# Optimization experiments

Measured on AMD Instinct MI355X. Metric: run time of the kernel, lower is better.

The kernel has to match this reference:

```python
import jax, jax.numpy as jnp
import numpy as np

N = 100000
IN_DIM = 256
HID = 256
EMB = 64
E = 3200000
EPS = 1e-3  # keras BatchNormalization default epsilon


def setup_inputs() -> dict:
    key = jax.random.key(0)
    ks = jax.random.split(key, 8)
    x = jax.random.normal(ks[0], (N, IN_DIM), dtype=jnp.float32)
    edge_row = jax.random.randint(ks[1], (E,), 0, N, dtype=jnp.int32)
    edge_col = jax.random.randint(ks[2], (E,), 0, N, dtype=jnp.int32)
    edge_val = jax.random.uniform(ks[3], (E,), dtype=jnp.float32)
    # glorot-uniform weights
    lim1 = float(np.sqrt(6.0 / (IN_DIM + HID)))
    w1 = jax.random.uniform(ks[4], (IN_DIM, HID), minval=-lim1, maxval=lim1, dtype=jnp.float32)
    lim2 = float(np.sqrt(6.0 / (HID + EMB)))
    w2 = jax.random.uniform(ks[5], (HID, EMB), minval=-lim2, maxval=lim2, dtype=jnp.float32)
    # BN params (inference mode uses moving stats)
    gamma1 = jnp.ones((HID,), jnp.float32)
    beta1 = jnp.zeros((HID,), jnp.float32)
    mean1 = jax.random.normal(ks[6], (HID,), dtype=jnp.float32) * 0.1
    var1 = jnp.ones((HID,), jnp.float32)
    gamma2 = jnp.ones((EMB,), jnp.float32)
    beta2 = jnp.zeros((EMB,), jnp.float32)
    mean2 = jax.random.normal(ks[7], (EMB,), dtype=jnp.float32) * 0.1
    var2 = jnp.ones((EMB,), jnp.float32)
    return dict(x=x, edge_row=edge_row, edge_col=edge_col, edge_val=edge_val,
                w1=w1, w2=w2, gamma1=gamma1, beta1=beta1, mean1=mean1, var1=var1,
                gamma2=gamma2, beta2=beta2, mean2=mean2, var2=var2)


def _spmm(edge_row, edge_col, edge_val, dense):
    # out[i] = sum_{e: row_e == i} val_e * dense[col_e]
    gathered = edge_val[:, None] * dense[edge_col]  # [E, D]
    return jax.ops.segment_sum(gathered, edge_row, num_segments=N)


def _bn_inf(h, gamma, beta, mean, var):
    return (h - mean) * jax.lax.rsqrt(var + EPS) * gamma + beta


def reference(x, edge_row, edge_col, edge_val, w1, w2,
              gamma1, beta1, mean1, var1, gamma2, beta2, mean2, var2):
    # layer 1: A @ (X W1), BN (inference), ReLU; dropout is identity at inference
    h = _spmm(edge_row, edge_col, edge_val, x @ w1)
    h = jax.nn.relu(_bn_inf(h, gamma1, beta1, mean1, var1))
    # layer 2
    z = _spmm(edge_row, edge_col, edge_val, h @ w2)
    z = _bn_inf(z, gamma2, beta2, mean2, var2)
    return z
```

## Files before the change

### kernel.cpp

```cpp
#include <hip/hip_runtime.h>
#include <hip/hip_bf16.h>

constexpr int NN   = 100000;
constexpr int IND  = 256;
constexpr int HIDD = 256;
constexpr int EMBD = 64;
constexpr int EE   = 3200000;
constexpr int CB    = 8;
constexpr int NB    = ((NN - 1) >> CB) + 1;
constexpr int NBP   = 512;
constexpr int CHUNK = 4096;
constexpr int EPT   = CHUNK / 256;
constexpr int NCHUNK = (EE + CHUNK - 1) / CHUNK;
constexpr int GMT    = 8;
constexpr int GROWS  = GMT * 16;
constexpr int GGRID  = (NN + GROWS - 1) / GROWS;
constexpr int APITCH = 264;
#define EPS_BN 1e-3f

typedef short  short8  __attribute__((ext_vector_type(8)));
typedef float  floatx4 __attribute__((ext_vector_type(4)));
typedef float  floatx2 __attribute__((ext_vector_type(2)));

static __device__ __forceinline__ unsigned short f2bf(float f) {
  __hip_bfloat16 b = __float2bfloat16(f);
  union { __hip_bfloat16 b; unsigned short u; } cv;
  cv.b = b;
  return cv.u;
}
static __device__ __forceinline__ float bf2f(unsigned short u) {
  return __uint_as_float(((unsigned)u) << 16);
}
static __device__ __forceinline__ unsigned char f2fp8(float f) {
  return (unsigned char)__builtin_amdgcn_cvt_pk_fp8_f32(f, f, 0, false);
}

__global__ __launch_bounds__(256) void swz_w1_kernel(
    const float* __restrict__ w1, unsigned short* __restrict__ w1s) {
  const int t = blockIdx.x * blockDim.x + threadIdx.x;
  const int lane = t & 63;
  const int f = t >> 6;
  const int kt = f >> 4;
  const int nt = f & 15;
  const int n = nt * 16 + (lane & 15);
#pragma unroll
  for (int j = 0; j < 8; ++j) {
    const int k = kt * 32 + (lane >> 4) * 8 + j;
    w1s[(size_t)(f * 64 + lane) * 8 + j] = f2bf(w1[k * HIDD + n]);
  }
}

__global__ __launch_bounds__(256) void swz_w2_kernel(
    const float* __restrict__ w2, unsigned short* __restrict__ w2s) {
  const int t = blockIdx.x * blockDim.x + threadIdx.x;
  const int lane = t & 63;
  const int f = t >> 6;
  const int kt = f >> 2;
  const int nt = f & 3;
  const int n = nt * 16 + (lane & 15);
#pragma unroll
  for (int j = 0; j < 8; ++j) {
    const int k = kt * 32 + (lane >> 4) * 8 + j;
    w2s[(size_t)(f * 64 + lane) * 8 + j] = f2bf(w2[k * EMBD + n]);
  }
}

__global__ __launch_bounds__(512) void gemm1_mfma(
    const float* __restrict__ x, const unsigned short* __restrict__ w1s,
    unsigned char* __restrict__ h0) {
  __shared__ unsigned short sa[2][16][APITCH];
  const int tid  = threadIdx.x;
  const int lane = tid & 63;
  const int wave = tid >> 6;
  const int quad = lane >> 4;
  const int l15  = lane & 15;
  const short8* w1v = (const short8*)w1s;
  short8 bf[2][8];
#pragma unroll
  for (int nt2 = 0; nt2 < 2; ++nt2)
#pragma unroll
    for (int kt = 0; kt < 8; ++kt)
      bf[nt2][kt] = w1v[(size_t)(kt * 16 + wave * 2 + nt2) * 64 + lane];

  const int mbase = blockIdx.x * GROWS;
  const int srow = tid >> 5;
  const int scol = (tid & 31) * 8;

  auto srcp = [&](int mt) -> const float* {
    int r = mbase + mt * 16 + srow;
    if (r >= NN) r = NN - 1;
    return x + (size_t)r * IND + scol;
  };

  {
    const float* p = srcp(0);
    float4 g0 = *(const float4*)(p);
    float4 g1 = *(const float4*)(p + 4);
    short8 s;
    s[0] = (short)f2bf(g0.x); s[1] = (short)f2bf(g0.y);
    s[2] = (short)f2bf(g0.z); s[3] = (short)f2bf(g0.w);
    s[4] = (short)f2bf(g1.x); s[5] = (short)f2bf(g1.y);
    s[6] = (short)f2bf(g1.z); s[7] = (short)f2bf(g1.w);
    *(short8*)&sa[0][srow][(tid & 31) * 8] = s;
  }

#pragma unroll
  for (int mt = 0; mt < GMT; ++mt) {
    const int cur = mt & 1;
    float4 g0, g1;
    if (mt + 1 < GMT) {
      const float* p = srcp(mt + 1);
      g0 = *(const float4*)(p);
      g1 = *(const float4*)(p + 4);
    }
    __syncthreads();
    floatx4 c0 = {0.f, 0.f, 0.f, 0.f};
    floatx4 c1 = {0.f, 0.f, 0.f, 0.f};
#pragma unroll
    for (int kt = 0; kt < 8; ++kt) {
      short8 a = *(const short8*)&sa[cur][l15][quad * 8 + kt * 32];
      c0 = __builtin_amdgcn_mfma_f32_16x16x32_bf16(a, bf[0][kt], c0, 0, 0, 0);
      c1 = __builtin_amdgcn_mfma_f32_16x16x32_bf16(a, bf[1][kt], c1, 0, 0, 0);
    }
    const int m0 = mbase + mt * 16;
    if (m0 < NN) {
      unsigned char* o = h0 + (size_t)(m0 + quad * 4) * HIDD + wave * 32 + l15;
#pragma unroll
      for (int r = 0; r < 4; ++r) {
        o[(size_t)r * HIDD]      = f2fp8(c0[r]);
        o[(size_t)r * HIDD + 16] = f2fp8(c1[r]);
      }
    }
    if (mt + 1 < GMT) {
      short8 s;
      s[0] = (short)f2bf(g0.x); s[1] = (short)f2bf(g0.y);
      s[2] = (short)f2bf(g0.z); s[3] = (short)f2bf(g0.w);
      s[4] = (short)f2bf(g1.x); s[5] = (short)f2bf(g1.y);
      s[6] = (short)f2bf(g1.z); s[7] = (short)f2bf(g1.w);
      *(short8*)&sa[cur ^ 1][srow][(tid & 31) * 8] = s;
    }
  }
}

__global__ __launch_bounds__(256) void gemm2_mfma(
    const unsigned short* __restrict__ hb, const unsigned short* __restrict__ w2s,
    unsigned char* __restrict__ z0) {
  __shared__ unsigned short sa[2][16][APITCH];
  const int tid  = threadIdx.x;
  const int lane = tid & 63;
  const int wave = tid >> 6;
  const int quad = lane >> 4;
  const int l15  = lane & 15;
  const short8* w2v = (const short8*)w2s;
  short8 bf[8];
#pragma unroll
  for (int kt = 0; kt < 8; ++kt)
    bf[kt] = w2v[(size_t)(kt * 4 + wave) * 64 + lane];

  const int mbase = blockIdx.x * GROWS;
  const int srow = tid >> 4;
  const int scol = (tid & 15) * 16;

  auto srcp = [&](int mt) -> const unsigned short* {
    int r = mbase + mt * 16 + srow;
    if (r >= NN) r = NN - 1;
    return hb + (size_t)r * HIDD + scol;
  };

  {
    const unsigned short* p = srcp(0);
    short8 g0 = *(const short8*)(p);
    short8 g1 = *(const short8*)(p + 8);
    *(short8*)&sa[0][srow][scol]     = g0;
    *(short8*)&sa[0][srow][scol + 8] = g1;
  }

#pragma unroll
  for (int mt = 0; mt < GMT; ++mt) {
    const int cur = mt & 1;
    short8 g0, g1;
    if (mt + 1 < GMT) {
      const unsigned short* p = srcp(mt + 1);
      g0 = *(const short8*)(p);
      g1 = *(const short8*)(p + 8);
    }
    __syncthreads();
    floatx4 c = {0.f, 0.f, 0.f, 0.f};
#pragma unroll
    for (int kt = 0; kt < 8; ++kt) {
      short8 a = *(const short8*)&sa[cur][l15][quad * 8 + kt * 32];
      c = __builtin_amdgcn_mfma_f32_16x16x32_bf16(a, bf[kt], c, 0, 0, 0);
    }
    const int m0 = mbase + mt * 16;
    if (m0 < NN) {
      unsigned char* o = z0 + (size_t)(m0 + quad * 4) * EMBD + wave * 16 + l15;
#pragma unroll
      for (int r = 0; r < 4; ++r) o[(size_t)r * EMBD] = f2fp8(c[r]);
    }
    if (mt + 1 < GMT) {
      *(short8*)&sa[cur ^ 1][srow][scol]     = g0;
      *(short8*)&sa[cur ^ 1][srow][scol + 8] = g1;
    }
  }
}

__global__ __launch_bounds__(256) void histb_kernel(
    const int* __restrict__ row, int* __restrict__ bcnt) {
  __shared__ int lcnt[NB];
  for (int i = threadIdx.x; i < NB; i += 256) lcnt[i] = 0;
  __syncthreads();
  const int base = blockIdx.x * CHUNK;
  const int lim  = min(EE - base, CHUNK);
  for (int i = threadIdx.x; i < lim; i += 256)
    atomicAdd(&lcnt[row[base + i] >> CB], 1);
  __syncthreads();
  for (int i = threadIdx.x; i < NB; i += 256) {
    const int c = lcnt[i];
    if (c) atomicAdd(&bcnt[i * 16], c);
  }
}

__global__ __launch_bounds__(512) void bscan_kernel(
    const int* __restrict__ bcnt, int* __restrict__ bucket_start,
    int* __restrict__ bcur) {
  __shared__ int lds[512];
  int v = (threadIdx.x < NB) ? bcnt[threadIdx.x * 16] : 0;
  lds[threadIdx.x] = v;
  for (int off = 1; off < 512; off <<= 1) {
    __syncthreads();
    int t = (threadIdx.x >= off) ? lds[threadIdx.x - off] : 0;
    __syncthreads();
    lds[threadIdx.x] += t;
  }
  __syncthreads();
  if (threadIdx.x < NB) {
    const int excl = lds[threadIdx.x] - v;
    bucket_start[threadIdx.x] = excl;
    bcur[threadIdx.x * 16] = excl;
  }
  if (threadIdx.x == 0) bucket_start[NB] = EE;
}

__global__ __launch_bounds__(256) void partA_kernel(
    const int* __restrict__ row, const int* __restrict__ col,
    const float* __restrict__ val, int* __restrict__ bcur,
    unsigned long long* __restrict__ staged) {
  __shared__ unsigned long long sbuf[CHUNK];
  __shared__ int cnt[NBP];
  __shared__ int scn[NBP];
  __shared__ int cur[NB];
  __shared__ int gofs[NB];
  const int base = blockIdx.x * CHUNK;
  const int lim  = min(EE - base, CHUNK);
  for (int i = threadIdx.x; i < NBP; i += 256) cnt[i] = 0;
  __syncthreads();
  unsigned long long rec[EPT];
  int bkt[EPT];
#pragma unroll
  for (int j = 0; j < EPT; ++j) {
    const int idx = threadIdx.x + j * 256;
    bkt[j] = -1;
    if (idx < lim) {
      const int e = base + idx;
      const int r = row[e];
      const int c = col[e];
      const unsigned short v = f2bf(val[e]);
      rec[j] = ((unsigned long long)r << 33) | ((unsigned long long)c << 16) | v;
      bkt[j] = r >> CB;
      atomicAdd(&cnt[bkt[j]], 1);
    }
  }
  __syncthreads();
  for (int i = threadIdx.x; i < NBP; i += 256) scn[i] = cnt[i];
  __syncthreads();
  for (int off = 1; off < NBP; off <<= 1) {
    const int i0 = threadIdx.x, i1 = threadIdx.x + 256;
    const int t0 = (i0 >= off) ? scn[i0 - off] : 0;
    const int t1 = (i1 >= off) ? scn[i1 - off] : 0;
    __syncthreads();
    scn[i0] += t0;
    scn[i1] += t1;
    __syncthreads();
  }
  for (int b = threadIdx.x; b < NB; b += 256) cur[b] = scn[b] - cnt[b];
  __syncthreads();
#pragma unroll
  for (int j = 0; j < EPT; ++j)
    if (bkt[j] >= 0) {
      const int p = atomicAdd(&cur[bkt[j]], 1);
      sbuf[p] = rec[j];
    }
  __syncthreads();
  for (int b = threadIdx.x; b < NB; b += 256) {
    const int c = cnt[b];
    const int g = (c > 0) ? atomicAdd(&bcur[b * 16], c) : 0;
    gofs[b] = g - (scn[b] - c);
  }
  __syncthreads();
  for (int s = threadIdx.x; s < lim; s += 256) {
    const unsigned long long rc = sbuf[s];
    const int b = (int)(rc >> (33 + CB));
    staged[(size_t)(gofs[b] + s)] = rc;
  }
}

__global__ __launch_bounds__(256) void partB_kernel(
    const int* __restrict__ bucket_start,
    const unsigned long long* __restrict__ staged,
    int2* __restrict__ edges, int* __restrict__ row_start) {
  __shared__ int cnt[1 << CB];
  __shared__ int ofs[1 << CB];
  const int b  = blockIdx.x;
  const int r0 = b << CB;
  const int rn = min(NN - r0, 1 << CB);
  const int s  = bucket_start[b];
  const int e  = bucket_start[b + 1];
  cnt[threadIdx.x] = 0;
  __syncthreads();
  const unsigned* hi = (const unsigned*)staged;
  for (int p = s + threadIdx.x; p < e; p += 256) {
    const unsigned hw = hi[2 * p + 1];
    const int r = (int)((hw >> 1) & 0x1FFFF);
    atomicAdd(&cnt[r - r0], 1);
  }
  __syncthreads();
  const int v = cnt[threadIdx.x];
  ofs[threadIdx.x] = v;
  for (int off = 1; off < 256; off <<= 1) {
    __syncthreads();
    const int t = (threadIdx.x >= off) ? ofs[threadIdx.x - off] : 0;
    __syncthreads();
    ofs[threadIdx.x] += t;
  }
  __syncthreads();
  const int excl = ofs[threadIdx.x] - v;
  if ((int)threadIdx.x < rn) row_start[r0 + threadIdx.x] = s + excl;
  if (b == NB - 1 && threadIdx.x == 0) row_start[NN] = e;
  __syncthreads();
  cnt[threadIdx.x] = s + excl;
  __syncthreads();
  for (int p = s + threadIdx.x; p < e; p += 256) {
    const unsigned long long rc = staged[p];
    const int r = (int)(rc >> 33);
    const int c = (int)((rc >> 16) & 0x1FFFF);
    const float vv = bf2f((unsigned short)(rc & 0xFFFF));
    const int q = atomicAdd(&cnt[r - r0], 1);
    int2 pk; pk.x = c << 6; pk.y = __float_as_int(vv);
    edges[q] = pk;
  }
}

__global__ __launch_bounds__(256, 8) void spmm1_kernel(
    const unsigned char* __restrict__ h0, const int* __restrict__ row_start,
    const int2* __restrict__ edges,
    const float* __restrict__ gamma, const float* __restrict__ beta,
    const float* __restrict__ mean, const float* __restrict__ var,
    unsigned short* __restrict__ h) {
  const int row  = (blockIdx.x * blockDim.x + threadIdx.x) >> 6;
  const int lane = threadIdx.x & 63;
  const int grp  = lane >> 4;
  const int t    = lane & 15;
  const int t16  = t * 16;
  const int s = row_start[row];
  const int e = row_start[row + 1];
  floatx2 acc[8];
#pragma unroll
  for (int j = 0; j < 8; ++j) acc[j] = floatx2{0.f, 0.f};

  const int ebulk = s + ((e - s) & ~15);
  int p = s;
  for (; p < ebulk; p += 16) {
    unsigned coff[4];
    float    vv4[4];
#pragma unroll
    for (int k = 0; k < 4; ++k) {
      const int2 er = edges[p + k * 4 + grp];
      coff[k] = (unsigned)er.x;
      vv4[k]  = __int_as_float(er.y);
    }
    uint4 gg[4];
#pragma unroll
    for (int k = 0; k < 4; ++k)
      gg[k] = *(const uint4*)(h0 + (size_t)coff[k] * 4 + t16);
#pragma unroll
    for (int k = 0; k < 4; ++k) {
      const floatx2 v2 = {vv4[k], vv4[k]};
      acc[0] += __builtin_amdgcn_cvt_pk_f32_fp8(gg[k].x, false) * v2;
      acc[1] += __builtin_amdgcn_cvt_pk_f32_fp8(gg[k].x, true)  * v2;
      acc[2] += __builtin_amdgcn_cvt_pk_f32_fp8(gg[k].y, false) * v2;
      acc[3] += __builtin_amdgcn_cvt_pk_f32_fp8(gg[k].y, true)  * v2;
      acc[4] += __builtin_amdgcn_cvt_pk_f32_fp8(gg[k].z, false) * v2;
      acc[5] += __builtin_amdgcn_cvt_pk_f32_fp8(gg[k].z, true)  * v2;
      acc[6] += __builtin_amdgcn_cvt_pk_f32_fp8(gg[k].w, false) * v2;
      acc[7] += __builtin_amdgcn_cvt_pk_f32_fp8(gg[k].w, true)  * v2;
    }
  }
  for (; p < e; p += 4) {
    const int idx = p + grp;
    const bool valid = idx < e;
    const int2 er = edges[valid ? idx : e - 1];
    const unsigned coff = (unsigned)er.x;
    const float vv = valid ? __int_as_float(er.y) : 0.f;
    const uint4 gg = *(const uint4*)(h0 + (size_t)coff * 4 + t16);
    const floatx2 v2 = {vv, vv};
    acc[0] += __builtin_amdgcn_cvt_pk_f32_fp8(gg.x, false) * v2;
    acc[1] += __builtin_amdgcn_cvt_pk_f32_fp8(gg.x, true)  * v2;
    acc[2] += __builtin_amdgcn_cvt_pk_f32_fp8(gg.y, false) * v2;
    acc[3] += __builtin_amdgcn_cvt_pk_f32_fp8(gg.y, true)  * v2;
    acc[4] += __builtin_amdgcn_cvt_pk_f32_fp8(gg.z, false) * v2;
    acc[5] += __builtin_amdgcn_cvt_pk_f32_fp8(gg.z, true)  * v2;
    acc[6] += __builtin_amdgcn_cvt_pk_f32_fp8(gg.w, false) * v2;
    acc[7] += __builtin_amdgcn_cvt_pk_f32_fp8(gg.w, true)  * v2;
  }
#pragma unroll
  for (int j = 0; j < 8; ++j) {
    acc[j][0] += __shfl_xor(acc[j][0], 16);
    acc[j][1] += __shfl_xor(acc[j][1], 16);
  }
#pragma unroll
  for (int j = 0; j < 8; ++j) {
    acc[j][0] += __shfl_xor(acc[j][0], 32);
    acc[j][1] += __shfl_xor(acc[j][1], 32);
  }
  floatx2 pa, pb;
  if (grp == 0)      { pa = acc[0]; pb = acc[1]; }
  else if (grp == 1) { pa = acc[2]; pb = acc[3]; }
  else if (grp == 2) { pa = acc[4]; pb = acc[5]; }
  else               { pa = acc[6]; pb = acc[7]; }
  const int d = t16 + grp * 4;
  float4 g  = *(const float4*)(gamma + d);
  float4 b  = *(const float4*)(beta + d);
  float4 m  = *(const float4*)(mean + d);
  float4 vv = *(const float4*)(var + d);
  const unsigned short o0 =
      f2bf(fmaxf(fmaf((pa[0] - m.x) * rsqrtf(vv.x + EPS_BN), g.x, b.x), 0.f));
  const unsigned short o1 =
      f2bf(fmaxf(fmaf((pa[1] - m.y) * rsqrtf(vv.y + EPS_BN), g.y, b.y), 0.f));
  const unsigned short o2 =
      f2bf(fmaxf(fmaf((pb[0] - m.z) * rsqrtf(vv.z + EPS_BN), g.z, b.z), 0.f));
  const unsigned short o3 =
      f2bf(fmaxf(fmaf((pb[1] - m.w) * rsqrtf(vv.w + EPS_BN), g.w, b.w), 0.f));
  const unsigned long long ow =
      (unsigned long long)o0 | ((unsigned long long)o1 << 16) |
      ((unsigned long long)o2 << 32) | ((unsigned long long)o3 << 48);
  __builtin_nontemporal_store(
      ow, (unsigned long long*)(h + (size_t)row * HIDD + d));
}

__global__ __launch_bounds__(256, 8) void spmm2_kernel(
    const unsigned char* __restrict__ z0, const int* __restrict__ row_start,
    const int2* __restrict__ edges,
    const float* __restrict__ gamma, const float* __restrict__ beta,
    const float* __restrict__ mean, const float* __restrict__ var,
    float* __restrict__ out) {
  const int row  = (blockIdx.x * blockDim.x + threadIdx.x) >> 6;
  const int lane = threadIdx.x & 63;
  const int grp  = lane >> 4;
  const int t    = lane & 15;
  const int t4   = t * 4;
  const int s = row_start[row];
  const int e = row_start[row + 1];
  floatx2 a01 = {0.f, 0.f};
  floatx2 a23 = {0.f, 0.f};
  const int ebulk = s + ((e - s) & ~15);
  int p = s;
  for (; p < ebulk; p += 16) {
    unsigned coff[4];
    float    vv4[4];
#pragma unroll
    for (int k = 0; k < 4; ++k) {
      const int2 er = edges[p + k * 4 + grp];
      coff[k] = (unsigned)er.x;
      vv4[k]  = __int_as_float(er.y);
    }
    unsigned gg[4];
#pragma unroll
    for (int k = 0; k < 4; ++k)
      gg[k] = *(const unsigned*)(z0 + (size_t)coff[k] + t4);
#pragma unroll
    for (int k = 0; k < 4; ++k) {
      const floatx2 v2 = {vv4[k], vv4[k]};
      a01 += __builtin_amdgcn_cvt_pk_f32_fp8(gg[k], false) * v2;
      a23 += __builtin_amdgcn_cvt_pk_f32_fp8(gg[k], true)  * v2;
    }
  }
  for (; p < e; p += 4) {
    const int idx = p + grp;
    const bool valid = idx < e;
    const int2 er = edges[valid ? idx : e - 1];
    const unsigned coff = (unsigned)er.x;
    const float vvs = valid ? __int_as_float(er.y) : 0.f;
    const unsigned gg = *(const unsigned*)(z0 + (size_t)coff + t4);
    const floatx2 v2 = {vvs, vvs};
    a01 += __builtin_amdgcn_cvt_pk_f32_fp8(gg, false) * v2;
    a23 += __builtin_amdgcn_cvt_pk_f32_fp8(gg, true)  * v2;
  }
  a01[0] += __shfl_xor(a01[0], 16); a01[1] += __shfl_xor(a01[1], 16);
  a23[0] += __shfl_xor(a23[0], 16); a23[1] += __shfl_xor(a23[1], 16);
  a01[0] += __shfl_xor(a01[0], 32); a01[1] += __shfl_xor(a01[1], 32);
  a23[0] += __shfl_xor(a23[0], 32); a23[1] += __shfl_xor(a23[1], 32);
  float av;
  if (grp == 0)      av = a01[0];
  else if (grp == 1) av = a01[1];
  else if (grp == 2) av = a23[0];
  else               av = a23[1];
  const int d = t4 + grp;
  const float r = fmaf((av - mean[d]) * rsqrtf(var[d] + EPS_BN), gamma[d],
                       beta[d]);
  __builtin_nontemporal_store(r, out + (size_t)row * EMBD + d);
}

extern "C" void kernel_launch(void* const* d_in, const int* in_sizes, int n_in,
                              void* d_out, int out_size, void* d_ws, size_t ws_size,
                              hipStream_t stream) {
  const float* x        = (const float*)d_in[0];
  const int*   edge_row = (const int*)d_in[1];
  const int*   edge_col = (const int*)d_in[2];
  const float* edge_val = (const float*)d_in[3];
  const float* w1       = (const float*)d_in[4];
  const float* w2       = (const float*)d_in[5];
  const float* gamma1   = (const float*)d_in[6];
  const float* beta1    = (const float*)d_in[7];
  const float* mean1    = (const float*)d_in[8];
  const float* var1     = (const float*)d_in[9];
  const float* gamma2   = (const float*)d_in[10];
  const float* beta2    = (const float*)d_in[11];
  const float* mean2    = (const float*)d_in[12];
  const float* var2     = (const float*)d_in[13];
  float* out = (float*)d_out;

  char* ws = (char*)d_ws;
  size_t off = 0;
  auto alloc = [&](size_t bytes) -> void* {
    void* p = ws + off;
    off = (off + bytes + 255) & ~(size_t)255;
    return p;
  };
  unsigned char*  h0  = (unsigned char*)alloc((size_t)NN * HIDD);
  unsigned short* h   = (unsigned short*)alloc((size_t)NN * HIDD * 2);
  unsigned long long* staged = (unsigned long long*)h;
  unsigned char*  z0  = (unsigned char*)alloc((size_t)NN * EMBD);
  unsigned short* w1s = (unsigned short*)alloc((size_t)IND * HIDD * 2);
  unsigned short* w2s = (unsigned short*)alloc((size_t)HIDD * EMBD * 2);
  int*   row_start    = (int*)alloc((size_t)(NN + 1) * 4);
  int*   bcnt         = (int*)alloc((size_t)NB * 16 * 4);
  int*   bcur         = (int*)alloc((size_t)NB * 16 * 4);
  int*   bucket_start = (int*)alloc((size_t)(NB + 1) * 4);
  int2*  edges        = (int2*)alloc((size_t)EE * 8);

  swz_w1_kernel<<<8192 / 256, 256, 0, stream>>>(w1, w1s);
  swz_w2_kernel<<<2048 / 256, 256, 0, stream>>>(w2, w2s);

  hipMemsetAsync(bcnt, 0, (size_t)NB * 16 * 4, stream);
  histb_kernel<<<NCHUNK, 256, 0, stream>>>(edge_row, bcnt);
  bscan_kernel<<<1, 512, 0, stream>>>(bcnt, bucket_start, bcur);
  partA_kernel<<<NCHUNK, 256, 0, stream>>>(
      edge_row, edge_col, edge_val, bcur, staged);
  partB_kernel<<<NB, 256, 0, stream>>>(bucket_start, staged, edges, row_start);

  gemm1_mfma<<<GGRID, 512, 0, stream>>>(x, w1s, h0);
  spmm1_kernel<<<NN / 4, 256, 0, stream>>>(h0, row_start, edges,
                                           gamma1, beta1, mean1, var1, h);
  gemm2_mfma<<<GGRID, 256, 0, stream>>>(h, w2s, z0);
  spmm2_kernel<<<NN / 4, 256, 0, stream>>>(z0, row_start, edges,
                                           gamma2, beta2, mean2, var2, out);
}
```

Measured before the change: 515.2 us.

## Fuse second-layer GEMM into first SpMM epilogue via shared-memory MFMA

The first SpMM kernel now has each wave aggregate four rows, apply BN+ReLU, and write bf16 results into a 16-row shared tile. The block then multiplies that tile by W2 with MFMA and writes fp8 z0 directly. This removes the separate gemm2 kernel and the round trip of the bf16 hidden matrix through global memory. The cost is lower occupancy (launch bound drops from 8 to 6, more registers held for W2 fragments) and serial per-wave row processing, which may hurt latency hiding in the gather.

```diff
diff --git a/kernel.cpp b/kernel.cpp
--- a/kernel.cpp
+++ b/kernel.cpp
@@ -142,68 +142,6 @@
   }
 }
 
-__global__ __launch_bounds__(256) void gemm2_mfma(
-    const unsigned short* __restrict__ hb, const unsigned short* __restrict__ w2s,
-    unsigned char* __restrict__ z0) {
-  __shared__ unsigned short sa[2][16][APITCH];
-  const int tid  = threadIdx.x;
-  const int lane = tid & 63;
-  const int wave = tid >> 6;
-  const int quad = lane >> 4;
-  const int l15  = lane & 15;
-  const short8* w2v = (const short8*)w2s;
-  short8 bf[8];
-#pragma unroll
-  for (int kt = 0; kt < 8; ++kt)
-    bf[kt] = w2v[(size_t)(kt * 4 + wave) * 64 + lane];
-
-  const int mbase = blockIdx.x * GROWS;
-  const int srow = tid >> 4;
-  const int scol = (tid & 15) * 16;
-
-  auto srcp = [&](int mt) -> const unsigned short* {
-    int r = mbase + mt * 16 + srow;
-    if (r >= NN) r = NN - 1;
-    return hb + (size_t)r * HIDD + scol;
-  };
-
-  {
-    const unsigned short* p = srcp(0);
-    short8 g0 = *(const short8*)(p);
-    short8 g1 = *(const short8*)(p + 8);
-    *(short8*)&sa[0][srow][scol]     = g0;
-    *(short8*)&sa[0][srow][scol + 8] = g1;
-  }
-
-#pragma unroll
-  for (int mt = 0; mt < GMT; ++mt) {
-    const int cur = mt & 1;
-    short8 g0, g1;
-    if (mt + 1 < GMT) {
-      const unsigned short* p = srcp(mt + 1);
-      g0 = *(const short8*)(p);
-      g1 = *(const short8*)(p + 8);
-    }
-    __syncthreads();
-    floatx4 c = {0.f, 0.f, 0.f, 0.f};
-#pragma unroll
-    for (int kt = 0; kt < 8; ++kt) {
-      short8 a = *(const short8*)&sa[cur][l15][quad * 8 + kt * 32];
-      c = __builtin_amdgcn_mfma_f32_16x16x32_bf16(a, bf[kt], c, 0, 0, 0);
-    }
-    const int m0 = mbase + mt * 16;
-    if (m0 < NN) {
-      unsigned char* o = z0 + (size_t)(m0 + quad * 4) * EMBD + wave * 16 + l15;
-#pragma unroll
-      for (int r = 0; r < 4; ++r) o[(size_t)r * EMBD] = f2fp8(c[r]);
-    }
-    if (mt + 1 < GMT) {
-      *(short8*)&sa[cur ^ 1][srow][scol]     = g0;
-      *(short8*)&sa[cur ^ 1][srow][scol + 8] = g1;
-    }
-  }
-}
-
 __global__ __launch_bounds__(256) void histb_kernel(
     const int* __restrict__ row, int* __restrict__ bcnt) {
   __shared__ int lcnt[NB];
@@ -350,101 +288,128 @@
   }
 }
 
-__global__ __launch_bounds__(256, 8) void spmm1_kernel(
+__global__ __launch_bounds__(256, 6) void spmm1_fused(
     const unsigned char* __restrict__ h0, const int* __restrict__ row_start,
     const int2* __restrict__ edges,
     const float* __restrict__ gamma, const float* __restrict__ beta,
     const float* __restrict__ mean, const float* __restrict__ var,
-    unsigned short* __restrict__ h) {
-  const int row  = (blockIdx.x * blockDim.x + threadIdx.x) >> 6;
+    const unsigned short* __restrict__ w2s, unsigned char* __restrict__ z0) {
+  __shared__ unsigned short sa[16][APITCH];
   const int lane = threadIdx.x & 63;
+  const int wave = threadIdx.x >> 6;
   const int grp  = lane >> 4;
   const int t    = lane & 15;
   const int t16  = t * 16;
-  const int s = row_start[row];
-  const int e = row_start[row + 1];
-  floatx2 acc[8];
-#pragma unroll
-  for (int j = 0; j < 8; ++j) acc[j] = floatx2{0.f, 0.f};
-
-  const int ebulk = s + ((e - s) & ~15);
-  int p = s;
-  for (; p < ebulk; p += 16) {
-    unsigned coff[4];
-    float    vv4[4];
-#pragma unroll
-    for (int k = 0; k < 4; ++k) {
-      const int2 er = edges[p + k * 4 + grp];
-      coff[k] = (unsigned)er.x;
-      vv4[k]  = __int_as_float(er.y);
-    }
-    uint4 gg[4];
-#pragma unroll
-    for (int k = 0; k < 4; ++k)
-      gg[k] = *(const uint4*)(h0 + (size_t)coff[k] * 4 + t16);
-#pragma unroll
-    for (int k = 0; k < 4; ++k) {
-      const floatx2 v2 = {vv4[k], vv4[k]};
-      acc[0] += __builtin_amdgcn_cvt_pk_f32_fp8(gg[k].x, false) * v2;
-      acc[1] += __builtin_amdgcn_cvt_pk_f32_fp8(gg[k].x, true)  * v2;
-      acc[2] += __builtin_amdgcn_cvt_pk_f32_fp8(gg[k].y, false) * v2;
-      acc[3] += __builtin_amdgcn_cvt_pk_f32_fp8(gg[k].y, true)  * v2;
-      acc[4] += __builtin_amdgcn_cvt_pk_f32_fp8(gg[k].z, false) * v2;
-      acc[5] += __builtin_amdgcn_cvt_pk_f32_fp8(gg[k].z, true)  * v2;
-      acc[6] += __builtin_amdgcn_cvt_pk_f32_fp8(gg[k].w, false) * v2;
-      acc[7] += __builtin_amdgcn_cvt_pk_f32_fp8(gg[k].w, true)  * v2;
-    }
-  }
-  for (; p < e; p += 4) {
-    const int idx = p + grp;
-    const bool valid = idx < e;
-    const int2 er = edges[valid ? idx : e - 1];
-    const unsigned coff = (unsigned)er.x;
-    const float vv = valid ? __int_as_float(er.y) : 0.f;
-    const uint4 gg = *(const uint4*)(h0 + (size_t)coff * 4 + t16);
-    const floatx2 v2 = {vv, vv};
-    acc[0] += __builtin_amdgcn_cvt_pk_f32_fp8(gg.x, false) * v2;
-    acc[1] += __builtin_amdgcn_cvt_pk_f32_fp8(gg.x, true)  * v2;
-    acc[2] += __builtin_amdgcn_cvt_pk_f32_fp8(gg.y, false) * v2;
-    acc[3] += __builtin_amdgcn_cvt_pk_f32_fp8(gg.y, true)  * v2;
-    acc[4] += __builtin_amdgcn_cvt_pk_f32_fp8(gg.z, false) * v2;
-    acc[5] += __builtin_amdgcn_cvt_pk_f32_fp8(gg.z, true)  * v2;
-    acc[6] += __builtin_amdgcn_cvt_pk_f32_fp8(gg.w, false) * v2;
-    acc[7] += __builtin_amdgcn_cvt_pk_f32_fp8(gg.w, true)  * v2;
-  }
-#pragma unroll
-  for (int j = 0; j < 8; ++j) {
-    acc[j][0] += __shfl_xor(acc[j][0], 16);
-    acc[j][1] += __shfl_xor(acc[j][1], 16);
-  }
-#pragma unroll
-  for (int j = 0; j < 8; ++j) {
-    acc[j][0] += __shfl_xor(acc[j][0], 32);
-    acc[j][1] += __shfl_xor(acc[j][1], 32);
-  }
-  floatx2 pa, pb;
-  if (grp == 0)      { pa = acc[0]; pb = acc[1]; }
-  else if (grp == 1) { pa = acc[2]; pb = acc[3]; }
-  else if (grp == 2) { pa = acc[4]; pb = acc[5]; }
-  else               { pa = acc[6]; pb = acc[7]; }
-  const int d = t16 + grp * 4;
+  const int d    = t16 + grp * 4;
+
+  const short8* w2v = (const short8*)w2s;
+  short8 bfr[8];
+#pragma unroll
+  for (int kt = 0; kt < 8; ++kt)
+    bfr[kt] = w2v[(size_t)(kt * 4 + wave) * 64 + lane];
+
   float4 g  = *(const float4*)(gamma + d);
   float4 b  = *(const float4*)(beta + d);
   float4 m  = *(const float4*)(mean + d);
   float4 vv = *(const float4*)(var + d);
-  const unsigned short o0 =
-      f2bf(fmaxf(fmaf((pa[0] - m.x) * rsqrtf(vv.x + EPS_BN), g.x, b.x), 0.f));
-  const unsigned short o1 =
-      f2bf(fmaxf(fmaf((pa[1] - m.y) * rsqrtf(vv.y + EPS_BN), g.y, b.y), 0.f));
-  const unsigned short o2 =
-      f2bf(fmaxf(fmaf((pb[0] - m.z) * rsqrtf(vv.z + EPS_BN), g.z, b.z), 0.f));
-  const unsigned short o3 =
-      f2bf(fmaxf(fmaf((pb[1] - m.w) * rsqrtf(vv.w + EPS_BN), g.w, b.w), 0.f));
-  const unsigned long long ow =
-      (unsigned long long)o0 | ((unsigned long long)o1 << 16) |
-      ((unsigned long long)o2 << 32) | ((unsigned long long)o3 << 48);
-  __builtin_nontemporal_store(
-      ow, (unsigned long long*)(h + (size_t)row * HIDD + d));
+  const float4 rs = {rsqrtf(vv.x + EPS_BN), rsqrtf(vv.y + EPS_BN),
+                     rsqrtf(vv.z + EPS_BN), rsqrtf(vv.w + EPS_BN)};
+
+  const int rbase = blockIdx.x * 16 + wave * 4;
+  for (int i = 0; i < 4; ++i) {
+    const int row = rbase + i;
+    const int s = row_start[row];
+    const int e = row_start[row + 1];
+    floatx2 acc[8];
+#pragma unroll
+    for (int j = 0; j < 8; ++j) acc[j] = floatx2{0.f, 0.f};
+
+    const int ebulk = s + ((e - s) & ~15);
+    int p = s;
+    for (; p < ebulk; p += 16) {
+      unsigned coff[4];
+      float    vv4[4];
+#pragma unroll
+      for (int k = 0; k < 4; ++k) {
+        const int2 er = edges[p + k * 4 + grp];
+        coff[k] = (unsigned)er.x;
+        vv4[k]  = __int_as_float(er.y);
+      }
+      uint4 gg[4];
+#pragma unroll
+      for (int k = 0; k < 4; ++k)
+        gg[k] = *(const uint4*)(h0 + (size_t)coff[k] * 4 + t16);
+#pragma unroll
+      for (int k = 0; k < 4; ++k) {
+        const floatx2 v2 = {vv4[k], vv4[k]};
+        acc[0] += __builtin_amdgcn_cvt_pk_f32_fp8(gg[k].x, false) * v2;
+        acc[1] += __builtin_amdgcn_cvt_pk_f32_fp8(gg[k].x, true)  * v2;
+        acc[2] += __builtin_amdgcn_cvt_pk_f32_fp8(gg[k].y, false) * v2;
+        acc[3] += __builtin_amdgcn_cvt_pk_f32_fp8(gg[k].y, true)  * v2;
+        acc[4] += __builtin_amdgcn_cvt_pk_f32_fp8(gg[k].z, false) * v2;
+        acc[5] += __builtin_amdgcn_cvt_pk_f32_fp8(gg[k].z, true)  * v2;
+        acc[6] += __builtin_amdgcn_cvt_pk_f32_fp8(gg[k].w, false) * v2;
+        acc[7] += __builtin_amdgcn_cvt_pk_f32_fp8(gg[k].w, true)  * v2;
+      }
+    }
+    for (; p < e; p += 4) {
+      const int idx = p + grp;
+      const bool valid = idx < e;
+      const int2 er = edges[valid ? idx : e - 1];
+      const unsigned coff = (unsigned)er.x;
+      const float vvs = valid ? __int_as_float(er.y) : 0.f;
+      const uint4 gg = *(const uint4*)(h0 + (size_t)coff * 4 + t16);
+      const floatx2 v2 = {vvs, vvs};
+      acc[0] += __builtin_amdgcn_cvt_pk_f32_fp8(gg.x, false) * v2;
+      acc[1] += __builtin_amdgcn_cvt_pk_f32_fp8(gg.x, true)  * v2;
+      acc[2] += __builtin_amdgcn_cvt_pk_f32_fp8(gg.y, false) * v2;
+      acc[3] += __builtin_amdgcn_cvt_pk_f32_fp8(gg.y, true)  * v2;
+      acc[4] += __builtin_amdgcn_cvt_pk_f32_fp8(gg.z, false) * v2;
+      acc[5] += __builtin_amdgcn_cvt_pk_f32_fp8(gg.z, true)  * v2;
+      acc[6] += __builtin_amdgcn_cvt_pk_f32_fp8(gg.w, false) * v2;
+      acc[7] += __builtin_amdgcn_cvt_pk_f32_fp8(gg.w, true)  * v2;
+    }
+#pragma unroll
+    for (int j = 0; j < 8; ++j) {
+      acc[j][0] += __shfl_xor(acc[j][0], 16);
+      acc[j][1] += __shfl_xor(acc[j][1], 16);
+    }
+#pragma unroll
+    for (int j = 0; j < 8; ++j) {
+      acc[j][0] += __shfl_xor(acc[j][0], 32);
+      acc[j][1] += __shfl_xor(acc[j][1], 32);
+    }
+    floatx2 pa, pb;
+    if (grp == 0)      { pa = acc[0]; pb = acc[1]; }
+    else if (grp == 1) { pa = acc[2]; pb = acc[3]; }
+    else if (grp == 2) { pa = acc[4]; pb = acc[5]; }
+    else               { pa = acc[6]; pb = acc[7]; }
+    const unsigned short o0 =
+        f2bf(fmaxf(fmaf((pa[0] - m.x) * rs.x, g.x, b.x), 0.f));
+    const unsigned short o1 =
+        f2bf(fmaxf(fmaf((pa[1] - m.y) * rs.y, g.y, b.y), 0.f));
+    const unsigned short o2 =
+        f2bf(fmaxf(fmaf((pb[0] - m.z) * rs.z, g.z, b.z), 0.f));
+    const unsigned short o3 =
+        f2bf(fmaxf(fmaf((pb[1] - m.w) * rs.w, g.w, b.w), 0.f));
+    const unsigned long long ow =
+        (unsigned long long)o0 | ((unsigned long long)o1 << 16) |
+        ((unsigned long long)o2 << 32) | ((unsigned long long)o3 << 48);
+    *(unsigned long long*)&sa[wave * 4 + i][d] = ow;
+  }
+  __syncthreads();
+  const int quad = grp;
+  const int l15  = t;
+  floatx4 c = {0.f, 0.f, 0.f, 0.f};
+#pragma unroll
+  for (int kt = 0; kt < 8; ++kt) {
+    short8 a = *(const short8*)&sa[l15][quad * 8 + kt * 32];
+    c = __builtin_amdgcn_mfma_f32_16x16x32_bf16(a, bfr[kt], c, 0, 0, 0);
+  }
+  const int m0 = blockIdx.x * 16;
+  unsigned char* o = z0 + (size_t)(m0 + quad * 4) * EMBD + wave * 16 + l15;
+#pragma unroll
+  for (int r = 0; r < 4; ++r) o[(size_t)r * EMBD] = f2fp8(c[r]);
 }
 
 __global__ __launch_bounds__(256, 8) void spmm2_kernel(
@@ -537,8 +502,8 @@
     return p;
   };
   unsigned char*  h0  = (unsigned char*)alloc((size_t)NN * HIDD);
-  unsigned short* h   = (unsigned short*)alloc((size_t)NN * HIDD * 2);
-  unsigned long long* staged = (unsigned long long*)h;
+  unsigned long long* staged =
+      (unsigned long long*)alloc((size_t)EE * 8);
   unsigned char*  z0  = (unsigned char*)alloc((size_t)NN * EMBD);
   unsigned short* w1s = (unsigned short*)alloc((size_t)IND * HIDD * 2);
   unsigned short* w2s = (unsigned short*)alloc((size_t)HIDD * EMBD * 2);
@@ -559,9 +524,9 @@
   partB_kernel<<<NB, 256, 0, stream>>>(bucket_start, staged, edges, row_start);
 
   gemm1_mfma<<<GGRID, 512, 0, stream>>>(x, w1s, h0);
-  spmm1_kernel<<<NN / 4, 256, 0, stream>>>(h0, row_start, edges,
-                                           gamma1, beta1, mean1, var1, h);
-  gemm2_mfma<<<GGRID, 256, 0, stream>>>(h, w2s, z0);
+  spmm1_fused<<<NN / 16, 256, 0, stream>>>(h0, row_start, edges,
+                                           gamma1, beta1, mean1, var1,
+                                           w2s, z0);
   spmm2_kernel<<<NN / 4, 256, 0, stream>>>(z0, row_start, edges,
                                            gamma2, beta2, mean2, var2, out);
 }
```

Result: slower. 566.9 us (+10.0%).

## Split spmm1 feature dimension into 8 column slabs across blocks

Applied to the files above, without the earlier changes.

spmm1 now launches 8x more blocks. Each block handles a 32-column slab of the 256-wide fp8 hidden features, with 8 lanes per edge and 8 edges in flight per wave, in place of one wave reading all 256 columns per edge. The aim is for each launch wave of blocks to touch only a slice of h0, so the random gathers stay resident in L2/LLC and get more parallelism. The cost is that edge lists and row_start are re-read 8 times, and the unrolled 16-edge bulk loop is dropped. Nontemporal stores in both spmm kernels are also replaced with plain stores.

```diff
diff --git a/kernel.cpp b/kernel.cpp
--- a/kernel.cpp
+++ b/kernel.cpp
@@ -16,6 +16,7 @@
 constexpr int GROWS  = GMT * 16;
 constexpr int GGRID  = (NN + GROWS - 1) / GROWS;
 constexpr int APITCH = 264;
+constexpr int NRB1   = NN / 4;
 #define EPS_BN 1e-3f
 
 typedef short  short8  __attribute__((ext_vector_type(8)));
@@ -356,95 +357,57 @@
     const float* __restrict__ gamma, const float* __restrict__ beta,
     const float* __restrict__ mean, const float* __restrict__ var,
     unsigned short* __restrict__ h) {
-  const int row  = (blockIdx.x * blockDim.x + threadIdx.x) >> 6;
+  const int sb   = blockIdx.x / NRB1;
+  const int rb   = blockIdx.x % NRB1;
   const int lane = threadIdx.x & 63;
-  const int grp  = lane >> 4;
-  const int t    = lane & 15;
-  const int t16  = t * 16;
+  const int wave = threadIdx.x >> 6;
+  const int grp8 = lane >> 3;
+  const int t8   = lane & 7;
+  const int doff = sb * 32 + t8 * 4;
+
+  const int row = rb * 4 + wave;
   const int s = row_start[row];
   const int e = row_start[row + 1];
-  floatx2 acc[8];
-#pragma unroll
-  for (int j = 0; j < 8; ++j) acc[j] = floatx2{0.f, 0.f};
-
-  const int ebulk = s + ((e - s) & ~15);
-  int p = s;
-  for (; p < ebulk; p += 16) {
-    unsigned coff[4];
-    float    vv4[4];
-#pragma unroll
-    for (int k = 0; k < 4; ++k) {
-      const int2 er = edges[p + k * 4 + grp];
-      coff[k] = (unsigned)er.x;
-      vv4[k]  = __int_as_float(er.y);
-    }
-    uint4 gg[4];
-#pragma unroll
-    for (int k = 0; k < 4; ++k)
-      gg[k] = *(const uint4*)(h0 + (size_t)coff[k] * 4 + t16);
-#pragma unroll
-    for (int k = 0; k < 4; ++k) {
-      const floatx2 v2 = {vv4[k], vv4[k]};
-      acc[0] += __builtin_amdgcn_cvt_pk_f32_fp8(gg[k].x, false) * v2;
-      acc[1] += __builtin_amdgcn_cvt_pk_f32_fp8(gg[k].x, true)  * v2;
-      acc[2] += __builtin_amdgcn_cvt_pk_f32_fp8(gg[k].y, false) * v2;
-      acc[3] += __builtin_amdgcn_cvt_pk_f32_fp8(gg[k].y, true)  * v2;
-      acc[4] += __builtin_amdgcn_cvt_pk_f32_fp8(gg[k].z, false) * v2;
-      acc[5] += __builtin_amdgcn_cvt_pk_f32_fp8(gg[k].z, true)  * v2;
-      acc[6] += __builtin_amdgcn_cvt_pk_f32_fp8(gg[k].w, false) * v2;
-      acc[7] += __builtin_amdgcn_cvt_pk_f32_fp8(gg[k].w, true)  * v2;
-    }
-  }
-  for (; p < e; p += 4) {
-    const int idx = p + grp;
+  const unsigned long long* e64 = (const unsigned long long*)edges;
+
+  floatx2 a01 = {0.f, 0.f};
+  floatx2 a23 = {0.f, 0.f};
+  for (int p = s; p < e; p += 8) {
+    const int idx = p + grp8;
     const bool valid = idx < e;
-    const int2 er = edges[valid ? idx : e - 1];
-    const unsigned coff = (unsigned)er.x;
-    const float vv = valid ? __int_as_float(er.y) : 0.f;
-    const uint4 gg = *(const uint4*)(h0 + (size_t)coff * 4 + t16);
-    const floatx2 v2 = {vv, vv};
-    acc[0] += __builtin_amdgcn_cvt_pk_f32_fp8(gg.x, false) * v2;
-    acc[1] += __builtin_amdgcn_cvt_pk_f32_fp8(gg.x, true)  * v2;
-    acc[2] += __builtin_amdgcn_cvt_pk_f32_fp8(gg.y, false) * v2;
-    acc[3] += __builtin_amdgcn_cvt_pk_f32_fp8(gg.y, true)  * v2;
-    acc[4] += __builtin_amdgcn_cvt_pk_f32_fp8(gg.z, false) * v2;
-    acc[5] += __builtin_amdgcn_cvt_pk_f32_fp8(gg.z, true)  * v2;
-    acc[6] += __builtin_amdgcn_cvt_pk_f32_fp8(gg.w, false) * v2;
-    acc[7] += __builtin_amdgcn_cvt_pk_f32_fp8(gg.w, true)  * v2;
-  }
-#pragma unroll
-  for (int j = 0; j < 8; ++j) {
-    acc[j][0] += __shfl_xor(acc[j][0], 16);
-    acc[j][1] += __shfl_xor(acc[j][1], 16);
-  }
-#pragma unroll
-  for (int j = 0; j < 8; ++j) {
-    acc[j][0] += __shfl_xor(acc[j][0], 32);
-    acc[j][1] += __shfl_xor(acc[j][1], 32);
-  }
-  floatx2 pa, pb;
-  if (grp == 0)      { pa = acc[0]; pb = acc[1]; }
-  else if (grp == 1) { pa = acc[2]; pb = acc[3]; }
-  else if (grp == 2) { pa = acc[4]; pb = acc[5]; }
-  else               { pa = acc[6]; pb = acc[7]; }
-  const int d = t16 + grp * 4;
-  float4 g  = *(const float4*)(gamma + d);
-  float4 b  = *(const float4*)(beta + d);
-  float4 m  = *(const float4*)(mean + d);
-  float4 vv = *(const float4*)(var + d);
-  const unsigned short o0 =
-      f2bf(fmaxf(fmaf((pa[0] - m.x) * rsqrtf(vv.x + EPS_BN), g.x, b.x), 0.f));
-  const unsigned short o1 =
-      f2bf(fmaxf(fmaf((pa[1] - m.y) * rsqrtf(vv.y + EPS_BN), g.y, b.y), 0.f));
-  const unsigned short o2 =
-      f2bf(fmaxf(fmaf((pb[0] - m.z) * rsqrtf(vv.z + EPS_BN), g.z, b.z), 0.f));
-  const unsigned short o3 =
-      f2bf(fmaxf(fmaf((pb[1] - m.w) * rsqrtf(vv.w + EPS_BN), g.w, b.w), 0.f));
-  const unsigned long long ow =
-      (unsigned long long)o0 | ((unsigned long long)o1 << 16) |
-      ((unsigned long long)o2 << 32) | ((unsigned long long)o3 << 48);
-  __builtin_nontemporal_store(
-      ow, (unsigned long long*)(h + (size_t)row * HIDD + d));
+    const unsigned long long rec = e64[valid ? idx : s];
+    const unsigned coff = (unsigned)(rec & 0xFFFFFFFFu);
+    const float v = valid ? __uint_as_float((unsigned)(rec >> 32)) : 0.f;
+    const unsigned g = *(const unsigned*)(h0 + (size_t)coff * 4 + doff);
+    const floatx2 v2 = {v, v};
+    a01 += __builtin_amdgcn_cvt_pk_f32_fp8(g, false) * v2;
+    a23 += __builtin_amdgcn_cvt_pk_f32_fp8(g, true)  * v2;
+  }
+  a01[0] += __shfl_xor(a01[0], 8);  a01[1] += __shfl_xor(a01[1], 8);
+  a23[0] += __shfl_xor(a23[0], 8);  a23[1] += __shfl_xor(a23[1], 8);
+  a01[0] += __shfl_xor(a01[0], 16); a01[1] += __shfl_xor(a01[1], 16);
+  a23[0] += __shfl_xor(a23[0], 16); a23[1] += __shfl_xor(a23[1], 16);
+  a01[0] += __shfl_xor(a01[0], 32); a01[1] += __shfl_xor(a01[1], 32);
+  a23[0] += __shfl_xor(a23[0], 32); a23[1] += __shfl_xor(a23[1], 32);
+  if (grp8 == 0) {
+    const int d = doff;
+    float4 g4 = *(const float4*)(gamma + d);
+    float4 b4 = *(const float4*)(beta + d);
+    float4 m4 = *(const float4*)(mean + d);
+    float4 v4 = *(const float4*)(var + d);
+    const unsigned short o0 =
+        f2bf(fmaxf(fmaf((a01[0] - m4.x) * rsqrtf(v4.x + EPS_BN), g4.x, b4.x), 0.f));
+    const unsigned short o1 =
+        f2bf(fmaxf(fmaf((a01[1] - m4.y) * rsqrtf(v4.y + EPS_BN), g4.y, b4.y), 0.f));
+    const unsigned short o2 =
+        f2bf(fmaxf(fmaf((a23[0] - m4.z) * rsqrtf(v4.z + EPS_BN), g4.z, b4.z), 0.f));
+    const unsigned short o3 =
+        f2bf(fmaxf(fmaf((a23[1] - m4.w) * rsqrtf(v4.w + EPS_BN), g4.w, b4.w), 0.f));
+    const unsigned long long ow =
+        (unsigned long long)o0 | ((unsigned long long)o1 << 16) |
+        ((unsigned long long)o2 << 32) | ((unsigned long long)o3 << 48);
+    *(unsigned long long*)(h + (size_t)row * HIDD + d) = ow;
+  }
 }
 
 __global__ __launch_bounds__(256, 8) void spmm2_kernel(
@@ -507,7 +470,7 @@
   const int d = t4 + grp;
   const float r = fmaf((av - mean[d]) * rsqrtf(var[d] + EPS_BN), gamma[d],
                        beta[d]);
-  __builtin_nontemporal_store(r, out + (size_t)row * EMBD + d);
+  out[(size_t)row * EMBD + d] = r;
 }
 
 extern "C" void kernel_launch(void* const* d_in, const int* in_sizes, int n_in,
@@ -559,8 +522,8 @@
   partB_kernel<<<NB, 256, 0, stream>>>(bucket_start, staged, edges, row_start);
 
   gemm1_mfma<<<GGRID, 512, 0, stream>>>(x, w1s, h0);
-  spmm1_kernel<<<NN / 4, 256, 0, stream>>>(h0, row_start, edges,
-                                           gamma1, beta1, mean1, var1, h);
+  spmm1_kernel<<<8 * NRB1, 256, 0, stream>>>(h0, row_start, edges,
+                                             gamma1, beta1, mean1, var1, h);
   gemm2_mfma<<<GGRID, 256, 0, stream>>>(h, w2s, z0);
   spmm2_kernel<<<NN / 4, 256, 0, stream>>>(z0, row_start, edges,
                                            gamma2, beta2, mean2, var2, out);
```

Result: slower. 884.0 us (+71.6%).

## Compute per-row CSR offsets via global row histogram and two-level scan

Applied to the files above, without the earlier changes.

Replaces the per-bucket LDS histogram with a per-row global-atomic histogram, followed by a two-level scan (per-bucket block scan plus bucket totals scan) and a finalize kernel that writes row_start. partB no longer re-reads the staged records to count rows and scan; it loads row_start directly. This removes one pass over the staged data in partB, at the cost of 3.2M scattered global atomics and two extra kernel launches.

```diff
diff --git a/kernel.cpp b/kernel.cpp
--- a/kernel.cpp
+++ b/kernel.cpp
@@ -204,31 +204,39 @@
   }
 }
 
-__global__ __launch_bounds__(256) void histb_kernel(
-    const int* __restrict__ row, int* __restrict__ bcnt) {
-  __shared__ int lcnt[NB];
-  for (int i = threadIdx.x; i < NB; i += 256) lcnt[i] = 0;
-  __syncthreads();
-  const int base = blockIdx.x * CHUNK;
-  const int lim  = min(EE - base, CHUNK);
-  for (int i = threadIdx.x; i < lim; i += 256)
-    atomicAdd(&lcnt[row[base + i] >> CB], 1);
-  __syncthreads();
-  for (int i = threadIdx.x; i < NB; i += 256) {
-    const int c = lcnt[i];
-    if (c) atomicAdd(&bcnt[i * 16], c);
-  }
-}
-
-__global__ __launch_bounds__(512) void bscan_kernel(
-    const int* __restrict__ bcnt, int* __restrict__ bucket_start,
+__global__ __launch_bounds__(256) void histr_kernel(
+    const int* __restrict__ row, int* __restrict__ cnt) {
+  const int i = blockIdx.x * 256 + threadIdx.x;
+  if (i < EE) atomicAdd(&cnt[row[i]], 1);
+}
+
+__global__ __launch_bounds__(256) void scanA_kernel(
+    const int* __restrict__ cnt, int* __restrict__ excl,
+    int* __restrict__ btot) {
+  __shared__ int lds[256];
+  const int r = blockIdx.x * 256 + threadIdx.x;
+  const int v = (r < NN) ? cnt[r] : 0;
+  lds[threadIdx.x] = v;
+  for (int off = 1; off < 256; off <<= 1) {
+    __syncthreads();
+    const int t = (threadIdx.x >= off) ? lds[threadIdx.x - off] : 0;
+    __syncthreads();
+    lds[threadIdx.x] += t;
+  }
+  __syncthreads();
+  if (r < NN) excl[r] = lds[threadIdx.x] - v;
+  if (threadIdx.x == 255) btot[blockIdx.x] = lds[255];
+}
+
+__global__ __launch_bounds__(512) void scanB_kernel(
+    const int* __restrict__ btot, int* __restrict__ bucket_start,
     int* __restrict__ bcur) {
   __shared__ int lds[512];
-  int v = (threadIdx.x < NB) ? bcnt[threadIdx.x * 16] : 0;
+  const int v = (threadIdx.x < NB) ? btot[threadIdx.x] : 0;
   lds[threadIdx.x] = v;
   for (int off = 1; off < 512; off <<= 1) {
     __syncthreads();
-    int t = (threadIdx.x >= off) ? lds[threadIdx.x - off] : 0;
+    const int t = (threadIdx.x >= off) ? lds[threadIdx.x - off] : 0;
     __syncthreads();
     lds[threadIdx.x] += t;
   }
@@ -239,6 +247,14 @@
     bcur[threadIdx.x * 16] = excl;
   }
   if (threadIdx.x == 0) bucket_start[NB] = EE;
+}
+
+__global__ __launch_bounds__(256) void fin_kernel(
+    const int* __restrict__ bucket_start, const int* __restrict__ excl,
+    int* __restrict__ row_start) {
+  const int r = blockIdx.x * 256 + threadIdx.x;
+  if (r < NN) row_start[r] = bucket_start[r >> CB] + excl[r];
+  if (r == 0) row_start[NN] = EE;
 }
 
 __global__ __launch_bounds__(256) void partA_kernel(
@@ -307,37 +323,14 @@
 __global__ __launch_bounds__(256) void partB_kernel(
     const int* __restrict__ bucket_start,
     const unsigned long long* __restrict__ staged,
-    int2* __restrict__ edges, int* __restrict__ row_start) {
+    const int* __restrict__ row_start, int2* __restrict__ edges) {
   __shared__ int cnt[1 << CB];
-  __shared__ int ofs[1 << CB];
   const int b  = blockIdx.x;
   const int r0 = b << CB;
   const int rn = min(NN - r0, 1 << CB);
   const int s  = bucket_start[b];
   const int e  = bucket_start[b + 1];
-  cnt[threadIdx.x] = 0;
-  __syncthreads();
-  const unsigned* hi = (const unsigned*)staged;
-  for (int p = s + threadIdx.x; p < e; p += 256) {
-    const unsigned hw = hi[2 * p + 1];
-    const int r = (int)((hw >> 1) & 0x1FFFF);
-    atomicAdd(&cnt[r - r0], 1);
-  }
-  __syncthreads();
-  const int v = cnt[threadIdx.x];
-  ofs[threadIdx.x] = v;
-  for (int off = 1; off < 256; off <<= 1) {
-    __syncthreads();
-    const int t = (threadIdx.x >= off) ? ofs[threadIdx.x - off] : 0;
-    __syncthreads();
-    ofs[threadIdx.x] += t;
-  }
-  __syncthreads();
-  const int excl = ofs[threadIdx.x] - v;
-  if ((int)threadIdx.x < rn) row_start[r0 + threadIdx.x] = s + excl;
-  if (b == NB - 1 && threadIdx.x == 0) row_start[NN] = e;
-  __syncthreads();
-  cnt[threadIdx.x] = s + excl;
+  cnt[threadIdx.x] = ((int)threadIdx.x < rn) ? row_start[r0 + threadIdx.x] : 0;
   __syncthreads();
   for (int p = s + threadIdx.x; p < e; p += 256) {
     const unsigned long long rc = staged[p];
@@ -543,7 +536,9 @@
   unsigned short* w1s = (unsigned short*)alloc((size_t)IND * HIDD * 2);
   unsigned short* w2s = (unsigned short*)alloc((size_t)HIDD * EMBD * 2);
   int*   row_start    = (int*)alloc((size_t)(NN + 1) * 4);
-  int*   bcnt         = (int*)alloc((size_t)NB * 16 * 4);
+  int*   cnt          = (int*)alloc((size_t)NN * 4);
+  int*   excl         = (int*)alloc((size_t)NN * 4);
+  int*   btot         = (int*)alloc((size_t)NB * 4);
   int*   bcur         = (int*)alloc((size_t)NB * 16 * 4);
   int*   bucket_start = (int*)alloc((size_t)(NB + 1) * 4);
   int2*  edges        = (int2*)alloc((size_t)EE * 8);
@@ -551,12 +546,14 @@
   swz_w1_kernel<<<8192 / 256, 256, 0, stream>>>(w1, w1s);
   swz_w2_kernel<<<2048 / 256, 256, 0, stream>>>(w2, w2s);
 
-  hipMemsetAsync(bcnt, 0, (size_t)NB * 16 * 4, stream);
-  histb_kernel<<<NCHUNK, 256, 0, stream>>>(edge_row, bcnt);
-  bscan_kernel<<<1, 512, 0, stream>>>(bcnt, bucket_start, bcur);
+  hipMemsetAsync(cnt, 0, (size_t)NN * 4, stream);
+  histr_kernel<<<(EE + 255) / 256, 256, 0, stream>>>(edge_row, cnt);
+  scanA_kernel<<<NB, 256, 0, stream>>>(cnt, excl, btot);
+  scanB_kernel<<<1, 512, 0, stream>>>(btot, bucket_start, bcur);
+  fin_kernel<<<NB, 256, 0, stream>>>(bucket_start, excl, row_start);
   partA_kernel<<<NCHUNK, 256, 0, stream>>>(
       edge_row, edge_col, edge_val, bcur, staged);
-  partB_kernel<<<NB, 256, 0, stream>>>(bucket_start, staged, edges, row_start);
+  partB_kernel<<<NB, 256, 0, stream>>>(bucket_start, staged, row_start, edges);
 
   gemm1_mfma<<<GGRID, 512, 0, stream>>>(x, w1s, h0);
   spmm1_kernel<<<NN / 4, 256, 0, stream>>>(h0, row_start, edges,
```

After: 610.2 us. +18.5%, slower.
